# Kernel tuning notes

Measured on AMD Instinct MI355X. Metric: run time of the kernel, lower is better.

The kernel has to match this reference:

```python
import jax, jax.numpy as jnp
import numpy as np

ALPHA = 0.2  # LeakyReLU negative slope
NEG_INF = -1e12


def setup_inputs() -> dict:
    key = jax.random.key(0)
    k1, k2, k3, k4 = jax.random.split(key, 4)
    B, N, F_in, F_out = 8, 4096, 128, 64
    inp = jax.random.normal(k1, (B, N, F_in), dtype=jnp.float32)
    adj = jax.random.randint(k2, (B, N, N), 0, 2, dtype=jnp.int32)
    # xavier-uniform-ish init for W, a
    W = jax.random.normal(k3, (F_in, F_out), dtype=jnp.float32) * (2.0 / (F_in + F_out)) ** 0.5
    a = jax.random.normal(k4, (2 * F_out, 1), dtype=jnp.float32) * (2.0 / (2 * F_out + 1)) ** 0.5
    return {"inp": inp, "adj": adj, "W": W, "a": a}


def reference(inp, adj, W, a):
    # inp: [B,N,F_in], adj: [B,N,N] int, W: [F_in,F_out], a: [2*F_out,1]
    F_out = W.shape[1]
    h = jnp.einsum('bnf,fo->bno', inp, W)          # [B,N,F_out]
    a1 = a[:F_out, 0]                              # [F_out]
    a2 = a[F_out:, 0]                              # [F_out]
    # e[b,i,j] = leakyrelu(h_i . a1 + h_j . a2)  (== concat([h_i,h_j]) @ a)
    s1 = h @ a1                                    # [B,N]
    s2 = h @ a2                                    # [B,N]
    e = s1[:, :, None] + s2[:, None, :]            # [B,N,N]
    e = jnp.where(e > 0, e, ALPHA * e)             # LeakyReLU
    att = jnp.where(adj > 0, e, NEG_INF)
    att = jax.nn.softmax(att, axis=-1)             # [B,N,N]
    # dropout p=0.0 -> identity
    h_prime = jnp.einsum('bij,bjo->bio', att, h)   # [B,N,F_out]
    return jax.nn.elu(h_prime)
```

## Files before the change

### kernel.cpp

```cpp
#include <hip/hip_runtime.h>
#include <hip/hip_bf16.h>
#include <hip/hip_fp16.h>
#include <cstdint>

typedef __attribute__((ext_vector_type(8))) short short8;
typedef __attribute__((ext_vector_type(4))) float floatx4;
typedef __attribute__((ext_vector_type(4))) int   intx4;

#define LEAKY_ALPHA 0.2f

__device__ __forceinline__ unsigned short f2bf_rne(float f) {
    unsigned u = __float_as_uint(f);
    unsigned r = u + 0x7FFFu + ((u >> 16) & 1u);
    return (unsigned short)(r >> 16);
}

__device__ __forceinline__ unsigned pk2bf(float lo, float hi) {
    union { __hip_bfloat162 b; unsigned u; } c;
    c.b = __float22bfloat162_rn(make_float2(lo, hi));
    return c.u;
}

__device__ __forceinline__ float2 h2f2(unsigned w) {
    union { unsigned u; __half2 h; } c; c.u = w;
    return __half22float2(c.h);
}


__global__ __launch_bounds__(256) void k_h(const float* __restrict__ inp,
                                           const float* __restrict__ W,
                                           const float* __restrict__ a,
                                           unsigned short* __restrict__ hT,
                                           float2* __restrict__ e1,
                                           __half2* __restrict__ e2h) {
    __shared__ float hs[64][65];
    const int tid  = threadIdx.x;
    const int wv   = tid >> 6;
    const int lane = tid & 63;
    const int blk  = blockIdx.x;
    const int b     = blk >> 6;
    const int ibase = (blk & 63) * 64;

    const float a1 = a[lane];
    const float a2 = a[64 + lane];

    for (int rr = 0; rr < 16; ++rr) {
        const int rloc = wv * 16 + rr;
        const int row  = ibase + rloc;
        const float* ip = inp + ((size_t)(b * 4096 + row)) * 128;
        float acc = 0.f;
        #pragma unroll
        for (int f = 0; f < 128; f += 4) {
            float4 v = *(const float4*)(ip + f);
            acc += v.x * W[(f + 0) * 64 + lane];
            acc += v.y * W[(f + 1) * 64 + lane];
            acc += v.z * W[(f + 2) * 64 + lane];
            acc += v.w * W[(f + 3) * 64 + lane];
        }
        hs[rloc][lane] = acc;
        float r1 = acc * a1;
        float r2 = acc * a2;
        #pragma unroll
        for (int off = 32; off > 0; off >>= 1) {
            r1 += __shfl_xor(r1, off);
            r2 += __shfl_xor(r2, off);
        }
        if (lane == 0) {
            e1[b * 4096 + row]  = make_float2(__expf(r1), __expf(LEAKY_ALPHA * r1));
            e2h[b * 4096 + row] = __floats2half2_rn(__expf(r2), __expf(LEAKY_ALPHA * r2));
        }
    }
    __syncthreads();

    const int o    = tid & 63;
    const int half = tid >> 6;
    const int tl   = half >> 1;
    const int nco  = (half & 1) * 16;
    unsigned pk[8];
    #pragma unroll
    for (int s = 0; s < 16; s += 2) {
        const int n0 = nco + s, n1 = nco + s + 1;
        const int c0 = 4 * (n0 & 7) + (n0 >> 3);
        const int c1 = 4 * (n1 & 7) + (n1 >> 3);
        unsigned lo = f2bf_rne(hs[tl * 32 + c0][o]);
        unsigned hi = f2bf_rne(hs[tl * 32 + c1][o]);
        pk[s >> 1] = lo | (hi << 16);
    }
    const int tile = (ibase >> 5) + tl;
    unsigned short* dst = hT + (((size_t)b * 128 + tile) * 64 + o) * 32 + nco;
    *(int4*)(dst)     = *(int4*)&pk[0];
    *(int4*)(dst + 8) = *(int4*)&pk[4];
}

__global__ __launch_bounds__(256, 4) void k_fused(const int* __restrict__ adj,
                                                  const unsigned short* __restrict__ hT,
                                                  const float2* __restrict__ e1g,
                                                  const __half2* __restrict__ e2hg,
                                                  float* __restrict__ out) {
    __shared__ unsigned long long mask64[32][16][4];
    __shared__ unsigned e2su[4096];

    const int tid   = threadIdx.x;
    const int b     = blockIdx.x >> 7;
    const int rtile = blockIdx.x & 127;
    const int wv    = tid >> 6;
    const int lane  = tid & 63;

    {
        const unsigned* src = (const unsigned*)(e2hg + b * 4096);
        #pragma unroll
        for (int t = 0; t < 4; ++t) {
            const int c0 = tid * 16 + t * 4;
            const int4 raw = *(const int4*)(src + c0);
            const int base = (c0 & ~31) + ((c0 & 31) >> 2);
            e2su[base +  0] = (unsigned)raw.x;
            e2su[base +  8] = (unsigned)raw.y;
            e2su[base + 16] = (unsigned)raw.z;
            e2su[base + 24] = (unsigned)raw.w;
        }
    }

    {
        const int* abase = adj + ((size_t)(b * 4096 + rtile * 32)) * 4096;
        for (int r = 0; r < 8; ++r) {
            const int lr = wv * 8 + r;
            const int* prow = abase + (size_t)lr * 4096 + lane * 4;
            #pragma unroll 4
            for (int g = 0; g < 16; ++g) {
                const intx4 v = __builtin_nontemporal_load((const intx4*)(prow + g * 256));
                const unsigned long long b0 = __ballot(v.x > 0);
                const unsigned long long b1 = __ballot(v.y > 0);
                const unsigned long long b2 = __ballot(v.z > 0);
                const unsigned long long b3 = __ballot(v.w > 0);
                if (lane == 0) {
                    ulonglong2* d = (ulonglong2*)&mask64[lr][g][0];
                    ulonglong2 t0; t0.x = b0; t0.y = b1;
                    ulonglong2 t1; t1.x = b2; t1.y = b3;
                    d[0] = t0; d[1] = t1;
                }
            }
        }
    }

    const int jhalf = wv >> 1;
    const int m     = lane & 15;
    const int kh    = lane >> 4;
    const int rl    = (wv & 1) * 16 + m;
    const int rbase = rtile * 32 + (wv & 1) * 16;
    const int row   = rbase + m;

    const float2 E1 = e1g[b * 4096 + row];
    const float E1p = E1.x, E1n = E1.y;
    const int jb0 = jhalf * 2048 + kh * 8;

    const unsigned short* hbase =
        hT + (((size_t)b * 128 + jhalf * 64) * 64 + m) * 32 + kh * 8;
    const unsigned short* hrow0 = hbase;
    const unsigned short* hrow1 = hbase + 512;
    const unsigned short* hrow2 = hbase + 1024;
    const unsigned short* hrow3 = hbase + 1536;

    floatx4 acc0 = (floatx4){0.f,0.f,0.f,0.f};
    floatx4 acc1 = (floatx4){0.f,0.f,0.f,0.f};
    floatx4 acc2 = (floatx4){0.f,0.f,0.f,0.f};
    floatx4 acc3 = (floatx4){0.f,0.f,0.f,0.f};
    float lsum = 0.f;

    short8 rb0_0, rb1_0, rb2_0, rb3_0, rb0_1, rb1_1, rb2_1, rb3_1;
    rb0_0 = *(const short8*)(hrow0);         rb1_0 = *(const short8*)(hrow1);
    rb2_0 = *(const short8*)(hrow2);         rb3_0 = *(const short8*)(hrow3);
    rb0_1 = *(const short8*)(hrow0 + 2048);  rb1_1 = *(const short8*)(hrow1 + 2048);
    rb2_1 = *(const short8*)(hrow2 + 2048);  rb3_1 = *(const short8*)(hrow3 + 2048);

    __syncthreads();

#define GAT_COL(WRD, T)                                                        \
    {                                                                          \
        const float2 ef = h2f2((unsigned)(WRD));                               \
        const float P  = E1p * ef.x;                                           \
        const float Nn = E1n * ef.y;                                           \
        float p = (P > 1.0f) ? P : Nn;                                         \
        p = ((mb >> (T)) & 1u) ? p : 0.0f;                                     \
        psum += p;                                                             \
        pv[T] = p;                                                             \
    }

#define GAT_STEP(SL, STEPIDX)                                                  \
    do {                                                                       \
        const short8 cb0 = rb0_##SL, cb1 = rb1_##SL;                           \
        const short8 cb2 = rb2_##SL, cb3 = rb3_##SL;                           \
        const int pstep = ((STEPIDX) + 2) & 63;         \
        const int poff = pstep * 2048;                         \
        rb0_##SL = *(const short8*)(hrow0 + poff);                             \
        rb1_##SL = *(const short8*)(hrow1 + poff);                             \
        rb2_##SL = *(const short8*)(hrow2 + poff);                             \
        rb3_##SL = *(const short8*)(hrow3 + poff);                             \
        const int soff = jb0 + (STEPIDX) * 32;                                 \
        const int4 eA = *(const int4*)&e2su[soff];                             \
        const int4 eB = *(const int4*)&e2su[soff + 4];                         \
        const unsigned mb = (unsigned)(Mcur >> (8 * ((STEPIDX) & 7))) & 0xffu; \
        float pv[8];                                                           \
        float psum = 0.f;                                                      \
        GAT_COL(eA.x, 0) GAT_COL(eA.y, 1) GAT_COL(eA.z, 2) GAT_COL(eA.w, 3)    \
        GAT_COL(eB.x, 4) GAT_COL(eB.y, 5) GAT_COL(eB.z, 6) GAT_COL(eB.w, 7)    \
        lsum += psum;                                                          \
        int4 ai;                                                               \
        ai.x = pk2bf(pv[0], pv[1]); ai.y = pk2bf(pv[2], pv[3]);                \
        ai.z = pk2bf(pv[4], pv[5]); ai.w = pk2bf(pv[6], pv[7]);                \
        union { int4 i; short8 s; } cc; cc.i = ai;                             \
        const short8 af = cc.s;                                                \
        acc0 = __builtin_amdgcn_mfma_f32_16x16x32_bf16(af, cb0, acc0, 0,0,0);  \
        acc1 = __builtin_amdgcn_mfma_f32_16x16x32_bf16(af, cb1, acc1, 0,0,0);  \
        acc2 = __builtin_amdgcn_mfma_f32_16x16x32_bf16(af, cb2, acc2, 0,0,0);  \
        acc3 = __builtin_amdgcn_mfma_f32_16x16x32_bf16(af, cb3, acc3, 0,0,0);  \
    } while (0)

    #pragma unroll 1
    for (int p = 0; p < 8; ++p) {
        const unsigned long long Mcur =
            *(const unsigned long long*)&mask64[rl][jhalf * 8 + p][kh];
        #pragma unroll
        for (int q = 0; q < 4; ++q) {
            GAT_STEP(0, p * 8 + 2 * q);
            GAT_STEP(1, p * 8 + 2 * q + 1);
        }
    }
#undef GAT_STEP
#undef GAT_COL

    lsum += __shfl_xor(lsum, 16);
    lsum += __shfl_xor(lsum, 32);

    floatx4 accs[4] = {acc0, acc1, acc2, acc3};

    float* accb = (float*)&mask64[0][0][0];
    float* lb   = accb + 2 * 64 * 17;

    __syncthreads();
    if (wv >= 2) {
        #pragma unroll
        for (int f = 0; f < 4; ++f)
            #pragma unroll
            for (int r = 0; r < 4; ++r)
                accb[(wv - 2) * 64 * 17 + lane * 17 + f * 4 + r] = accs[f][r];
        lb[(wv - 2) * 64 + lane] = lsum;
    }
    __syncthreads();
    if (wv < 2) {
        const float ltot = lsum + lb[wv * 64 + lane];
        #pragma unroll
        for (int f = 0; f < 4; ++f) {
            #pragma unroll
            for (int r = 0; r < 4; ++r) {
                float v = accs[f][r] + accb[wv * 64 * 17 + lane * 17 + f * 4 + r];
                const int drow = (lane >> 4) * 4 + r;
                const float lr = __shfl(ltot, drow);
                const float hp = v / lr;
                const float o  = (hp > 0.f) ? hp : (__expf(hp) - 1.f);
                out[((size_t)(b * 4096 + rbase + drow)) * 64 + f * 16 + (lane & 15)] = o;
            }
        }
    }
}

extern "C" void kernel_launch(void* const* d_in, const int* in_sizes, int n_in,
                              void* d_out, int out_size, void* d_ws, size_t ws_size,
                              hipStream_t stream) {
    const float* inp = (const float*)d_in[0];
    const int*   adj = (const int*)d_in[1];
    const float* W   = (const float*)d_in[2];
    const float* a   = (const float*)d_in[3];
    float* out = (float*)d_out;

    unsigned short* hT = (unsigned short*)d_ws;
    float2*  e1  = (float2*)((char*)d_ws + (size_t)4 * 1024 * 1024);
    __half2* e2h = (__half2*)((char*)d_ws + (size_t)4 * 1024 * 1024 + 262144);

    k_h<<<512, 256, 0, stream>>>(inp, W, a, hT, e1, e2h);
    k_fused<<<1024, 256, 0, stream>>>(adj, hT, e1, e2h, out);
}
```

Measured before the change: 791.9 us.

## Split adjacency bitmask packing into a separate streaming kernel

Moves the conversion of the int32 adjacency matrix into per-row bitmasks out of the fused attention kernel and into its own k_pack kernel. k_pack streams all of adj with many small waves, and the attention kernel then copies a compact precomputed mask into shared memory. The goal is to let the bandwidth-bound 512 MB adj read run at full occupancy, separate from the compute-heavy attention kernel with its lower occupancy. The cost is an extra kernel launch and a round trip of the 16 MB mask through global memory.

```diff
diff --git a/kernel.cpp b/kernel.cpp
--- a/kernel.cpp
+++ b/kernel.cpp
@@ -26,6 +26,29 @@
     return __half22float2(c.h);
 }
 
+
+__global__ __launch_bounds__(256, 8) void k_pack(const int* __restrict__ adj,
+                                                 ulonglong2* __restrict__ maskg) {
+    const int wid  = (int)((blockIdx.x * 256 + threadIdx.x) >> 6);
+    const int lane = threadIdx.x & 63;
+    const int* p0 = adj + (size_t)wid * 256 + lane * 4;
+    ulonglong2* m0 = maskg + (size_t)wid * 2;
+    #pragma unroll 2
+    for (int it = 0; it < 64; ++it) {
+        const intx4 v = __builtin_nontemporal_load(
+            (const intx4*)(p0 + (size_t)it * 8192 * 256));
+        const unsigned long long b0 = __ballot(v.x > 0);
+        const unsigned long long b1 = __ballot(v.y > 0);
+        const unsigned long long b2 = __ballot(v.z > 0);
+        const unsigned long long b3 = __ballot(v.w > 0);
+        if (lane == 0) {
+            ulonglong2 t0; t0.x = b0; t0.y = b1;
+            ulonglong2 t1; t1.x = b2; t1.y = b3;
+            ulonglong2* d = m0 + (size_t)it * 8192 * 2;
+            d[0] = t0; d[1] = t1;
+        }
+    }
+}
 
 __global__ __launch_bounds__(256) void k_h(const float* __restrict__ inp,
                                            const float* __restrict__ W,
@@ -92,11 +115,11 @@
     *(int4*)(dst + 8) = *(int4*)&pk[4];
 }
 
-__global__ __launch_bounds__(256, 4) void k_fused(const int* __restrict__ adj,
-                                                  const unsigned short* __restrict__ hT,
-                                                  const float2* __restrict__ e1g,
-                                                  const __half2* __restrict__ e2hg,
-                                                  float* __restrict__ out) {
+__global__ __launch_bounds__(256, 4) void k_attn(const ulonglong2* __restrict__ maskg,
+                                                 const unsigned short* __restrict__ hT,
+                                                 const float2* __restrict__ e1g,
+                                                 const __half2* __restrict__ e2hg,
+                                                 float* __restrict__ out) {
     __shared__ unsigned long long mask64[32][16][4];
     __shared__ unsigned e2su[4096];
 
@@ -119,26 +142,13 @@
             e2su[base + 24] = (unsigned)raw.w;
         }
     }
-
     {
-        const int* abase = adj + ((size_t)(b * 4096 + rtile * 32)) * 4096;
-        for (int r = 0; r < 8; ++r) {
-            const int lr = wv * 8 + r;
-            const int* prow = abase + (size_t)lr * 4096 + lane * 4;
-            #pragma unroll 4
-            for (int g = 0; g < 16; ++g) {
-                const intx4 v = __builtin_nontemporal_load((const intx4*)(prow + g * 256));
-                const unsigned long long b0 = __ballot(v.x > 0);
-                const unsigned long long b1 = __ballot(v.y > 0);
-                const unsigned long long b2 = __ballot(v.z > 0);
-                const unsigned long long b3 = __ballot(v.w > 0);
-                if (lane == 0) {
-                    ulonglong2* d = (ulonglong2*)&mask64[lr][g][0];
-                    ulonglong2 t0; t0.x = b0; t0.y = b1;
-                    ulonglong2 t1; t1.x = b2; t1.y = b3;
-                    d[0] = t0; d[1] = t1;
-                }
-            }
+        const ulonglong2* gm = maskg + (size_t)(b * 4096 + rtile * 32) * 32;
+        ulonglong2* lm = (ulonglong2*)&mask64[0][0][0];
+        #pragma unroll
+        for (int q = 0; q < 4; ++q) {
+            const int idx = tid + q * 256;
+            lm[idx] = gm[idx];
         }
     }
 
@@ -275,7 +285,9 @@
     unsigned short* hT = (unsigned short*)d_ws;
     float2*  e1  = (float2*)((char*)d_ws + (size_t)4 * 1024 * 1024);
     __half2* e2h = (__half2*)((char*)d_ws + (size_t)4 * 1024 * 1024 + 262144);
-
+    ulonglong2* maskg = (ulonglong2*)((char*)d_ws + (size_t)6 * 1024 * 1024);
+
+    k_pack<<<2048, 256, 0, stream>>>(adj, maskg);
     k_h<<<512, 256, 0, stream>>>(inp, W, a, hT, e1, e2h);
-    k_fused<<<1024, 256, 0, stream>>>(adj, hT, e1, e2h, out);
-}
+    k_attn<<<1024, 256, 0, stream>>>(maskg, hT, e1, e2h, out);
+}
```

Measured after the change: 811.3 us. 2.4% more time.
